# Performance work log

Measured on AMD Instinct MI355X. Metric: run time of the kernel, lower is better.

The kernel has to match this reference:

```python
import jax, jax.numpy as jnp
import numpy as np

N_HEAD = 16
HEAD_DIM = 64
R_VALUE = 256
EPS_LN = 1e-5


def _orf(x, omega, b):
    # orthogonal random features: sqrt(2/r) * cos(x @ omega.T + b)
    r = b.shape[0]
    return jnp.sqrt(2.0 / r) * jnp.cos(x @ omega.T + b)


def _layernorm(x, gamma, beta):
    m = jnp.mean(x, axis=-1, keepdims=True)
    v = jnp.var(x, axis=-1, keepdims=True)
    return (x - m) / jnp.sqrt(v + EPS_LN) * gamma + beta


def setup_inputs() -> dict:
    key = jax.random.key(0)
    ks = jax.random.split(key, 12)
    B, L = 4, 2048
    dm = N_HEAD * HEAD_DIM  # 1024
    inp = {}
    inp["pre_query"] = jax.random.normal(ks[0], (B, L, dm), jnp.float32)
    inp["pre_key"] = jax.random.normal(ks[1], (B, L, dm), jnp.float32)
    inp["pre_value"] = jax.random.normal(ks[2], (B, L, dm), jnp.float32)
    inp["wq"] = jax.random.normal(ks[3], (dm, dm), jnp.float32) * 0.02
    inp["wk"] = jax.random.normal(ks[4], (dm, dm), jnp.float32) * 0.02
    inp["wv"] = jax.random.normal(ks[5], (dm, dm), jnp.float32) * 0.02
    inp["wo"] = jax.random.normal(ks[6], (dm, dm), jnp.float32) * 0.02
    inp["gamma"] = jnp.ones((dm,), jnp.float32)
    inp["beta"] = jnp.zeros((dm,), jnp.float32)
    G = jax.random.normal(ks[7], (R_VALUE, HEAD_DIM), jnp.float32)
    omega, _ = jnp.linalg.qr(G)  # (r, head_dim), orthonormal columns
    inp["omega"] = omega
    inp["b"] = jax.random.uniform(ks[8], (R_VALUE,), jnp.float32) * 2.0 * jnp.pi
    return inp


def reference(pre_query, pre_key, pre_value, wq, wk, wv, wo, gamma, beta, omega, b):
    B, L, dm = pre_query.shape
    H, D = N_HEAD, dm // N_HEAD
    q = (pre_query @ wq.T).reshape(B, L, H, D)
    k = (pre_key @ wk.T).reshape(B, L, H, D)
    v = (pre_value @ wv.T).reshape(B, L, H, D)

    qp = _orf(q, omega, b)  # (B,L,H,R)
    kp = _orf(k, omega, b)  # (B,L,H,R)

    # causal Performer attention as a linear-attention recurrence:
    # S_t = S_{t-1} + k'_t v_t^T ; z_t = z_{t-1} + k'_t
    # out_t = (q'_t . S_t) / clamp(q'_t . z_t)
    R = b.shape[0]
    S0 = jnp.zeros((B, H, R, D), qp.dtype)
    z0 = jnp.zeros((B, H, R), qp.dtype)

    def step(carry, xs):
        S, z = carry
        q_t, k_t, v_t = xs  # (B,H,R),(B,H,R),(B,H,D)
        S = S + k_t[..., :, None] * v_t[..., None, :]
        z = z + k_t
        num = jnp.einsum('bhr,bhrd->bhd', q_t, S)
        den = jnp.clip(jnp.einsum('bhr,bhr->bh', q_t, z), 1e-6, None)
        return (S, z), num / (den[..., None] + 1e-6)

    xs = (qp.transpose(1, 0, 2, 3), kp.transpose(1, 0, 2, 3), v.transpose(1, 0, 2, 3))
    _, out = jax.lax.scan(step, (S0, z0), xs)  # (L,B,H,D)
    out = out.transpose(1, 0, 2, 3).reshape(B, L, dm)

    pre_result = out @ wo.T
    return _layernorm(pre_result + pre_query, gamma, beta)
```

## Files before the change

kernel.cpp:

```cpp
#include <hip/hip_runtime.h>
#include <hip/hip_bf16.h>


typedef float f4 __attribute__((ext_vector_type(4)));
typedef __attribute__((ext_vector_type(8))) short bf16x8;
typedef __attribute__((ext_vector_type(4))) float f32x4;
typedef unsigned short u16x4 __attribute__((ext_vector_type(4)));
typedef unsigned short u16x8 __attribute__((ext_vector_type(8)));

#define B_  4
#define L_  2048
#define H_  16
#define D_  64
#define DM_ 1024
#define R_  256
#define C_  64
#define NC_ (L_ / C_)
#define M_  (B_ * L_)
#define M2_ (M_ * H_)

static __device__ __forceinline__ unsigned short f2bu(float x) {
    __hip_bfloat16 h = __float2bfloat16(x);
    return *(unsigned short*)&h;
}
static __device__ __forceinline__ float bu2f(unsigned short u) {
    union { unsigned int i; float f; } c; c.i = ((unsigned int)u) << 16; return c.f;
}

typedef __attribute__((address_space(3))) void lds_void_t;
typedef __attribute__((address_space(1))) const void gvoid_t;
static __device__ __forceinline__ void gload16(const void* g, void* l) {
    __builtin_amdgcn_global_load_lds((gvoid_t*)g, (lds_void_t*)l, 16, 0, 0);
}

__launch_bounds__(256)
__global__ void cvt_bf16(const float* __restrict__ in, unsigned short* __restrict__ out, int n4) {
    int i = blockIdx.x * 256 + threadIdx.x;
    if (i < n4) {
        f4 v = *(const f4*)&in[(size_t)i * 4];
        ushort4 o;
        o.x = f2bu(v[0]); o.y = f2bu(v[1]); o.z = f2bu(v[2]); o.w = f2bu(v[3]);
        *(ushort4*)&out[(size_t)i * 4] = o;
    }
}

__launch_bounds__(256)
__global__ void cvt_bf16_x3(const float* __restrict__ i0, const float* __restrict__ i1,
                            const float* __restrict__ i2,
                            unsigned short* __restrict__ o0, unsigned short* __restrict__ o1,
                            unsigned short* __restrict__ o2, int n4) {
    const int z = blockIdx.z;
    const float* in = (z == 0) ? i0 : (z == 1) ? i1 : i2;
    unsigned short* out = (z == 0) ? o0 : (z == 1) ? o1 : o2;
    int i = blockIdx.x * 256 + threadIdx.x;
    if (i < n4) {
        f4 v = *(const f4*)&in[(size_t)i * 4];
        ushort4 o;
        o.x = f2bu(v[0]); o.y = f2bu(v[1]); o.z = f2bu(v[2]); o.w = f2bu(v[3]);
        *(ushort4*)&out[(size_t)i * 4] = o;
    }
}

__launch_bounds__(512)
__global__ void gemm_mfma_b3(const unsigned short* __restrict__ A0, const unsigned short* __restrict__ A1,
                             const unsigned short* __restrict__ A2,
                             const unsigned short* __restrict__ B0, const unsigned short* __restrict__ B1,
                             const unsigned short* __restrict__ B2,
                             unsigned short* __restrict__ C0, unsigned short* __restrict__ C1,
                             unsigned short* __restrict__ C2,
                             int M, int N, int K) {
    __shared__ unsigned short Asl[2][256 * 32];
    __shared__ unsigned short Bsl[2][256 * 32];
    const int z = blockIdx.z;
    const unsigned short* A  = (z == 0) ? A0 : (z == 1) ? A1 : A2;
    const unsigned short* Bw = (z == 0) ? B0 : (z == 1) ? B1 : B2;
    unsigned short*       Cb = (z == 0) ? C0 : (z == 1) ? C1 : C2;
    const int t = threadIdx.x;
    const int lane = t & 63, w = t >> 6;
    const int wr = w >> 2, wc = w & 3;
    const int nwg = gridDim.x * gridDim.y;
    const int bid = blockIdx.y * gridDim.x + blockIdx.x;
    const int cpx = nwg >> 3;
    const int swz = (bid & 7) * cpx + (bid >> 3);
    const int row0 = (swz / gridDim.x) * 256, col0 = (swz % gridDim.x) * 256;
    const int sr0 = t >> 2;
    const int ssw = (((t & 3) ^ ((t >> 3) & 3)) * 8);
    const int lg = lane >> 4, lr = lane & 15;
    const int aslot = (lg ^ ((lr >> 1) & 3)) * 8;

#define STAGE_B3(buf, kkk) do { \
        gload16(&A [(size_t)(row0 + sr0)       * K + (kkk) + ssw], &Asl[buf][t * 8]); \
        gload16(&A [(size_t)(row0 + sr0 + 128) * K + (kkk) + ssw], &Asl[buf][(t + 512) * 8]); \
        gload16(&Bw[(size_t)(col0 + sr0)       * K + (kkk) + ssw], &Bsl[buf][t * 8]); \
        gload16(&Bw[(size_t)(col0 + sr0 + 128) * K + (kkk) + ssw], &Bsl[buf][(t + 512) * 8]); \
    } while (0)

    f32x4 acc[8][4] = {};
    STAGE_B3(0, 0);
    int cur = 0;
    for (int kk = 0; kk < K; kk += 32) {
        if (kk + 32 < K) {
            STAGE_B3(cur ^ 1, kk + 32);
            asm volatile("s_waitcnt vmcnt(4)" ::: "memory");
        } else {
            asm volatile("s_waitcnt vmcnt(0)" ::: "memory");
        }
        __builtin_amdgcn_sched_barrier(0);
        __builtin_amdgcn_s_barrier();
        bf16x8 af[8], bfr[4];
#pragma unroll
        for (int m = 0; m < 8; ++m)
            af[m] = *(const bf16x8*)&Asl[cur][(wr * 128 + m * 16 + lr) * 32 + aslot];
#pragma unroll
        for (int n = 0; n < 4; ++n)
            bfr[n] = *(const bf16x8*)&Bsl[cur][(wc * 64 + n * 16 + lr) * 32 + aslot];
        __builtin_amdgcn_s_setprio(1);
#pragma unroll
        for (int m = 0; m < 8; ++m)
#pragma unroll
            for (int n = 0; n < 4; ++n)
                acc[m][n] = __builtin_amdgcn_mfma_f32_16x16x32_bf16(af[m], bfr[n], acc[m][n], 0, 0, 0);
        __builtin_amdgcn_s_setprio(0);
        __builtin_amdgcn_s_barrier();
        cur ^= 1;
    }
#undef STAGE_B3
#pragma unroll
    for (int m = 0; m < 8; ++m)
#pragma unroll
        for (int n = 0; n < 4; ++n)
#pragma unroll
            for (int i = 0; i < 4; ++i) {
                int r  = row0 + wr * 128 + m * 16 + lg * 4 + i;
                int cc = col0 + wc * 64 + n * 16 + lr;
                Cb[(size_t)r * N + cc] = f2bu(acc[m][n][i]);
            }
}

__launch_bounds__(256)
__global__ void gemm_out(const unsigned short* __restrict__ A,
                         const unsigned short* __restrict__ Bw,
                         const float* __restrict__ resid,
                         float* __restrict__ Cf,
                         int M, int N, int K) {
    __shared__ unsigned short Asl[3][64 * 32];
    __shared__ unsigned short Bsl[3][128 * 32];
    const int t = threadIdx.x;
    const int lane = t & 63, w = t >> 6;
    const int nwg = gridDim.x * gridDim.y;
    const int bid = blockIdx.y * gridDim.x + blockIdx.x;
    const int cpx = nwg >> 3;
    const int swz = (bid & 7) * cpx + (bid >> 3);
    const int row0 = (swz / gridDim.x) * 64, col0 = (swz % gridDim.x) * 128;
    const int sr0 = t >> 2;
    const int ssw = (((t & 3) ^ ((t >> 3) & 3)) * 8);
    const int lg = lane >> 4, lr = lane & 15;
    const int aslot = (lg ^ ((lr >> 1) & 3)) * 8;

#define STAGE_O(buf, kkk) do { \
        gload16(&A [(size_t)(row0 + sr0)      * K + (kkk) + ssw], &Asl[buf][t * 8]); \
        gload16(&Bw[(size_t)(col0 + sr0)      * K + (kkk) + ssw], &Bsl[buf][t * 8]); \
        gload16(&Bw[(size_t)(col0 + sr0 + 64) * K + (kkk) + ssw], &Bsl[buf][(t + 256) * 8]); \
    } while (0)
#define COMPUTE_O(buf) do { \
        bf16x8 af[4], bfr[2]; \
        _Pragma("unroll") \
        for (int m = 0; m < 4; ++m) \
            af[m] = *(const bf16x8*)&Asl[buf][(m * 16 + lr) * 32 + aslot]; \
        _Pragma("unroll") \
        for (int n = 0; n < 2; ++n) \
            bfr[n] = *(const bf16x8*)&Bsl[buf][(w * 32 + n * 16 + lr) * 32 + aslot]; \
        _Pragma("unroll") \
        for (int m = 0; m < 4; ++m) \
            _Pragma("unroll") \
            for (int n = 0; n < 2; ++n) \
                acc[m][n] = __builtin_amdgcn_mfma_f32_16x16x32_bf16(af[m], bfr[n], acc[m][n], 0, 0, 0); \
    } while (0)

    f32x4 acc[4][2] = {};
    STAGE_O(0, 0);
    STAGE_O(1, 32);
    int cur = 0;
    for (int kk = 0; kk + 64 < K; kk += 32) {
        int nx = cur + 2; if (nx >= 3) nx -= 3;
        STAGE_O(nx, kk + 64);
        asm volatile("s_waitcnt vmcnt(6)" ::: "memory");
        __builtin_amdgcn_sched_barrier(0);
        __builtin_amdgcn_s_barrier();
        COMPUTE_O(cur);
        __builtin_amdgcn_s_barrier();
        cur = (cur == 2) ? 0 : cur + 1;
    }
    asm volatile("s_waitcnt vmcnt(3)" ::: "memory");
    __builtin_amdgcn_sched_barrier(0);
    __builtin_amdgcn_s_barrier();
    COMPUTE_O(cur);
    __builtin_amdgcn_s_barrier();
    cur = (cur == 2) ? 0 : cur + 1;
    asm volatile("s_waitcnt vmcnt(0)" ::: "memory");
    __builtin_amdgcn_sched_barrier(0);
    __builtin_amdgcn_s_barrier();
    COMPUTE_O(cur);
#undef STAGE_O
#undef COMPUTE_O
#pragma unroll
    for (int m = 0; m < 4; ++m)
#pragma unroll
        for (int n = 0; n < 2; ++n)
#pragma unroll
            for (int i = 0; i < 4; ++i) {
                int r  = row0 + m * 16 + lg * 4 + i;
                int cc = col0 + w * 32 + n * 16 + lr;
                size_t off = (size_t)r * N + cc;
                Cf[off] = acc[m][n][i] + resid[off];
            }
}

#define RS_STRIDE 272
__launch_bounds__(256)
__global__ void feat_mfma_b2(const unsigned short* __restrict__ X0, const unsigned short* __restrict__ X1,
                             const unsigned short* __restrict__ om,
                             const float* __restrict__ bvec,
                             unsigned short* __restrict__ O0, unsigned short* __restrict__ O1) {
    __shared__ unsigned short Xs[2 * 64 * 32];
    __shared__ unsigned short Pool[64 * RS_STRIDE];
    const int z = blockIdx.z;
    const unsigned short* X = z ? X1 : X0;
    unsigned short* out = z ? O1 : O0;
    const int t = threadIdx.x;
    const int lane = t & 63, w = t >> 6;
    const int lg = lane >> 4, lr = lane & 15;
    const int m0 = blockIdx.x * 64;
    const int aslot = (lg ^ ((lr >> 1) & 3)) * 8;

#pragma unroll
    for (int i = 0; i < 2; ++i) {
        int cch = i * 256 + t;
        int ks = cch >> 8, row = (cch >> 2) & 63;
        int sub = ((cch & 3) ^ ((cch >> 3) & 3)) * 8;
        gload16(&X[(size_t)(m0 + row) * 64 + ks * 32 + sub], &Xs[cch * 8]);
    }
#pragma unroll
    for (int i = 0; i < 8; ++i) {
        int cch = i * 256 + t;
        int ks = cch >> 10, r = (cch >> 2) & 255;
        int sub = ((cch & 3) ^ ((cch >> 3) & 3)) * 8;
        gload16(&om[(size_t)r * 64 + ks * 32 + sub], &Pool[cch * 8]);
    }
    __syncthreads();

    f32x4 acc[4][4] = {};
#pragma unroll
    for (int ks = 0; ks < 2; ++ks) {
        bf16x8 af[4], bfr[4];
#pragma unroll
        for (int m = 0; m < 4; ++m)
            af[m] = *(const bf16x8*)&Xs[ks * 2048 + (m * 16 + lr) * 32 + aslot];
#pragma unroll
        for (int n = 0; n < 4; ++n)
            bfr[n] = *(const bf16x8*)&Pool[ks * 8192 + (w * 64 + n * 16 + lr) * 32 + aslot];
#pragma unroll
        for (int m = 0; m < 4; ++m)
#pragma unroll
            for (int n = 0; n < 4; ++n)
                acc[m][n] = __builtin_amdgcn_mfma_f32_16x16x32_bf16(af[m], bfr[n], acc[m][n], 0, 0, 0);
    }
    __syncthreads();

    const float scale = 0.08838834764831845f;
#pragma unroll
    for (int n = 0; n < 4; ++n) {
        const int col = w * 64 + n * 16 + lr;
        const float bb = bvec[col];
#pragma unroll
        for (int m = 0; m < 4; ++m)
#pragma unroll
            for (int ii = 0; ii < 4; ++ii)
                Pool[(m * 16 + lg * 4 + ii) * RS_STRIDE + col] = f2bu(scale * __cosf(acc[m][n][ii] + bb));
    }
    __syncthreads();
#pragma unroll
    for (int i = 0; i < 8; ++i) {
        int cch = i * 256 + t;
        int row = cch >> 5, colc = (cch & 31) * 8;
        u16x8 vv = *(const u16x8*)&Pool[row * RS_STRIDE + colc];
        *(u16x8*)&out[(size_t)(m0 + row) * 256 + colc] = vv;
    }
}

__launch_bounds__(256)
__global__ void passA_mfma(const unsigned short* __restrict__ kp, const unsigned short* __restrict__ vb,
                           unsigned short* __restrict__ kvT, float* __restrict__ ksum) {
    __shared__ __align__(16) unsigned short KPt[256][72];
    __shared__ __align__(16) unsigned short Vt[64][72];
    const int c = blockIdx.x, h = blockIdx.y, bz = blockIdx.z;
    const int t = threadIdx.x;
    const int lane = t & 63, w = t >> 6;
    const int lg = lane >> 4, lr = lane & 15;
    const int l0 = c * C_;
    const int bh = bz * H_ + h;

    {
        const int l4 = (t & 15) * 4, rs = (t >> 4) * 16;
        u16x8 row[4][2];
#pragma unroll
        for (int i = 0; i < 4; ++i) {
            const unsigned short* src = &kp[((size_t)(bz * L_ + l0 + l4 + i) * H_ + h) * R_ + rs];
            row[i][0] = *(const u16x8*)src;
            row[i][1] = *(const u16x8*)(src + 8);
        }
#pragma unroll
        for (int q = 0; q < 16; ++q) {
            u16x4 pk = { row[0][q >> 3][q & 7], row[1][q >> 3][q & 7],
                         row[2][q >> 3][q & 7], row[3][q >> 3][q & 7] };
            *(u16x4*)&KPt[rs + q][l4] = pk;
        }
    }
    {
        const int d4 = (t & 15) * 4, ls = (t >> 4) * 4;
        u16x4 x[4];
#pragma unroll
        for (int i = 0; i < 4; ++i)
            x[i] = *(const u16x4*)&vb[(size_t)(bz * L_ + l0 + ls + i) * DM_ + h * 64 + d4];
#pragma unroll
        for (int q = 0; q < 4; ++q) {
            u16x4 pk = { x[0][q], x[1][q], x[2][q], x[3][q] };
            *(u16x4*)&Vt[d4 + q][ls] = pk;
        }
    }
    __syncthreads();

    f32x4 acc[4][4] = {};
#pragma unroll
    for (int ks = 0; ks < 2; ++ks) {
        bf16x8 af[4], bfr[4];
#pragma unroll
        for (int m = 0; m < 4; ++m)
            af[m] = *(const bf16x8*)&KPt[64 * w + 16 * m + lr][ks * 32 + lg * 8];
#pragma unroll
        for (int n = 0; n < 4; ++n)
            bfr[n] = *(const bf16x8*)&Vt[16 * n + lr][ks * 32 + lg * 8];
#pragma unroll
        for (int m = 0; m < 4; ++m)
#pragma unroll
            for (int n = 0; n < 4; ++n)
                acc[m][n] = __builtin_amdgcn_mfma_f32_16x16x32_bf16(af[m], bfr[n], acc[m][n], 0, 0, 0);
    }
    size_t sbase = ((size_t)(bh * NC_ + c)) * 64 * R_;
#pragma unroll
    for (int n = 0; n < 4; ++n)
#pragma unroll
        for (int m = 0; m < 4; ++m) {
            int d = 16 * n + lr;
            int r = 64 * w + 16 * m + lg * 4;
            u16x4 pk = { f2bu(acc[m][n][0]), f2bu(acc[m][n][1]),
                         f2bu(acc[m][n][2]), f2bu(acc[m][n][3]) };
            *(u16x4*)&kvT[sbase + (size_t)d * R_ + r] = pk;
        }
    {
        float s = 0.f;
#pragma unroll
        for (int j = 0; j < 8; ++j) {
            u16x8 vv = *(const u16x8*)&KPt[t][j * 8];
#pragma unroll
            for (int q = 0; q < 8; ++q) s += bu2f(vv[q]);
        }
        ksum[((size_t)(bh * NC_ + c)) * R_ + t] = s;
    }
}

__launch_bounds__(256)
__global__ void passB_chain(unsigned short* __restrict__ kvT, float* __restrict__ ksum) {
    const int bx = blockIdx.x, h = blockIdx.y, bz = blockIdx.z;
    const int t = threadIdx.x;
    const int bh = bz * H_ + h;
    const int idx = bx * 256 + t;
    const int d = idx >> 6;
    const int rg = (idx & 63) * 4;
    size_t base = ((size_t)bh * NC_ * 64 + d) * R_ + rg;
    const size_t cstride = (size_t)64 * R_;
    float run0 = 0.f, run1 = 0.f, run2 = 0.f, run3 = 0.f;
    for (int c = 0; c < NC_; ++c) {
        size_t ix = base + (size_t)c * cstride;
        u16x4 v = *(const u16x4*)&kvT[ix];
        u16x4 o = { f2bu(run0), f2bu(run1), f2bu(run2), f2bu(run3) };
        *(u16x4*)&kvT[ix] = o;
        run0 += bu2f(v[0]); run1 += bu2f(v[1]);
        run2 += bu2f(v[2]); run3 += bu2f(v[3]);
    }
    if (bx == 0) {
        float rz = 0.f;
        for (int c = 0; c < NC_; ++c) {
            size_t ix = ((size_t)bh * NC_ + c) * R_ + t;
            float tmp = ksum[ix];
            ksum[ix] = rz;
            rz += tmp;
        }
    }
}

__launch_bounds__(256)
__global__ void passC_mfma(const unsigned short* __restrict__ qp, const unsigned short* __restrict__ kp,
                           const unsigned short* __restrict__ vb, const unsigned short* __restrict__ kvT,
                           const float* __restrict__ zpref, unsigned short* __restrict__ attnb) {
    __shared__ __align__(16) unsigned short Sl[64 * 256];
    __shared__ __align__(16) unsigned short Vt[80][72];
    __shared__ __align__(16) unsigned short As[64][72];

    const int c = blockIdx.x, h = blockIdx.y, bz = blockIdx.z;
    const int t = threadIdx.x;
    const int lane = t & 63, w = t >> 6;
    const int lg = lane >> 4, lr = lane & 15;
    const int l0 = c * C_;
    const int bh = bz * H_ + h;
    const size_t sbase = ((size_t)(bh * NC_ + c)) * 64 * R_;
    const size_t zbase = ((size_t)(bh * NC_ + c)) * R_;

#pragma unroll
    for (int i = 0; i < 8; ++i) {
        int idx = i * 256 + t;
        int row = idx >> 5, s = idx & 31;
        gload16(&kvT[sbase + (size_t)row * R_ + ((s ^ (row & 7)) << 3)], &Sl[idx * 8]);
    }

    {
        const int d4 = (t & 15) * 4, ls = (t >> 4) * 4;
        u16x4 x[4];
#pragma unroll
        for (int i = 0; i < 4; ++i)
            x[i] = *(const u16x4*)&vb[(size_t)(bz * L_ + l0 + ls + i) * DM_ + h * 64 + d4];
#pragma unroll
        for (int q = 0; q < 4; ++q) {
            u16x4 pk = { x[0][q], x[1][q], x[2][q], x[3][q] };
            *(u16x4*)&Vt[d4 + q][ls] = pk;
        }
    }
    if (t < 16) {
        u16x4 ones = { 0x3F80, 0x3F80, 0x3F80, 0x3F80 };
        *(u16x4*)&Vt[64][t * 4] = ones;
    }

    const size_t qrow = ((size_t)(bz * L_ + l0 + 16 * w + lr) * H_ + h) * R_;
    bf16x8 aq[8];
#pragma unroll
    for (int ks = 0; ks < 8; ++ks) aq[ks] = *(const bf16x8*)&qp[qrow + ks * 32 + lg * 8];

    f32x4 sacc[4] = {};
#pragma unroll
    for (int half = 0; half < 2; ++half) {
        bf16x8 bk[4][4];
#pragma unroll
        for (int k2 = 0; k2 < 4; ++k2)
#pragma unroll
            for (int n = 0; n < 4; ++n)
                bk[k2][n] = *(const bf16x8*)&kp[((size_t)(bz * L_ + l0 + 16 * n + lr) * H_ + h) * R_
                                                + (half * 4 + k2) * 32 + lg * 8];
        __builtin_amdgcn_s_setprio(1);
#pragma unroll
        for (int k2 = 0; k2 < 4; ++k2)
#pragma unroll
            for (int n = 0; n < 4; ++n)
                sacc[n] = __builtin_amdgcn_mfma_f32_16x16x32_bf16(aq[half * 4 + k2], bk[k2][n], sacc[n], 0, 0, 0);
        __builtin_amdgcn_s_setprio(0);
    }
#pragma unroll
    for (int n = 0; n < 4; ++n)
#pragma unroll
        for (int ii = 0; ii < 4; ++ii) {
            int i_loc = 16 * w + lg * 4 + ii;
            int j_loc = 16 * n + lr;
            As[i_loc][j_loc] = (j_loc <= i_loc) ? f2bu(sacc[n][ii]) : (unsigned short)0;
        }

    u16x8 zu[8];
#pragma unroll
    for (int ks = 0; ks < 8; ++ks) {
        f4 z0 = *(const f4*)&zpref[zbase + ks * 32 + lg * 8];
        f4 z1 = *(const f4*)&zpref[zbase + ks * 32 + lg * 8 + 4];
        zu[ks] = u16x8{ f2bu(z0[0]), f2bu(z0[1]), f2bu(z0[2]), f2bu(z0[3]),
                        f2bu(z1[0]), f2bu(z1[1]), f2bu(z1[2]), f2bu(z1[3]) };
    }
    __syncthreads();

    f32x4 oacc[4] = {};
    f32x4 dacc = {};
    __builtin_amdgcn_s_setprio(1);
#pragma unroll
    for (int ks = 0; ks < 8; ++ks) {
#pragma unroll
        for (int n = 0; n < 4; ++n) {
            int row = 16 * n + lr;
            int slot = (ks * 4 + lg) ^ (lr & 7);
            bf16x8 bs = *(const bf16x8*)&Sl[row * 256 + slot * 8];
            oacc[n] = __builtin_amdgcn_mfma_f32_16x16x32_bf16(aq[ks], bs, oacc[n], 0, 0, 0);
        }
        dacc = __builtin_amdgcn_mfma_f32_16x16x32_bf16(aq[ks], *(bf16x8*)&zu[ks], dacc, 0, 0, 0);
    }

    f32x4 racc = {};
#pragma unroll
    for (int ks = 0; ks < 2; ++ks) {
        bf16x8 aa = *(const bf16x8*)&As[16 * w + lr][ks * 32 + lg * 8];
#pragma unroll
        for (int n = 0; n < 4; ++n) {
            bf16x8 bv = *(const bf16x8*)&Vt[16 * n + lr][ks * 32 + lg * 8];
            oacc[n] = __builtin_amdgcn_mfma_f32_16x16x32_bf16(aa, bv, oacc[n], 0, 0, 0);
        }
        bf16x8 b4 = *(const bf16x8*)&Vt[64 + lr][ks * 32 + lg * 8];
        racc = __builtin_amdgcn_mfma_f32_16x16x32_bf16(aa, b4, racc, 0, 0, 0);
    }
    __builtin_amdgcn_s_setprio(0);

#pragma unroll
    for (int ii = 0; ii < 4; ++ii) {
        float rs_ = __shfl(racc[ii], lane & 48, 64);
        float den = rs_ + dacc[ii];
        float inv = 1.f / (fmaxf(den, 1e-6f) + 1e-6f);
#pragma unroll
        for (int n = 0; n < 4; ++n)
            attnb[(size_t)(bz * L_ + l0 + 16 * w + lg * 4 + ii) * DM_ + h * 64 + 16 * n + lr] =
                f2bu(oacc[n][ii] * inv);
    }
}

__launch_bounds__(256)
__global__ void ln_kernel(float* __restrict__ io, const float* __restrict__ gamma,
                          const float* __restrict__ beta) {
    __shared__ float wsum[4], wsum2[4];
    const int row = blockIdx.x;
    const int t = threadIdx.x;
    f4 x = *(const f4*)&io[(size_t)row * DM_ + t * 4];
    float s  = x[0] + x[1] + x[2] + x[3];
    float s2 = x[0]*x[0] + x[1]*x[1] + x[2]*x[2] + x[3]*x[3];
#pragma unroll
    for (int o = 32; o > 0; o >>= 1) {
        s  += __shfl_down(s, o);
        s2 += __shfl_down(s2, o);
    }
    if ((t & 63) == 0) { wsum[t >> 6] = s; wsum2[t >> 6] = s2; }
    __syncthreads();
    s  = wsum[0]  + wsum[1]  + wsum[2]  + wsum[3];
    s2 = wsum2[0] + wsum2[1] + wsum2[2] + wsum2[3];
    const float m = s * (1.f / DM_);
    const float var = s2 * (1.f / DM_) - m * m;
    const float rstd = rsqrtf(var + 1e-5f);
    f4 g  = *(const f4*)&gamma[t * 4];
    f4 bb = *(const f4*)&beta[t * 4];
    f4 o = (x - m) * rstd * g + bb;
    *(f4*)&io[(size_t)row * DM_ + t * 4] = o;
}

extern "C" void kernel_launch(void* const* d_in, const int* in_sizes, int n_in,
                              void* d_out, int out_size, void* d_ws, size_t ws_size,
                              hipStream_t stream) {
    const float* pre_q = (const float*)d_in[0];
    const float* pre_k = (const float*)d_in[1];
    const float* pre_v = (const float*)d_in[2];
    const float* wq    = (const float*)d_in[3];
    const float* wk    = (const float*)d_in[4];
    const float* wv    = (const float*)d_in[5];
    const float* wo    = (const float*)d_in[6];
    const float* gamma = (const float*)d_in[7];
    const float* beta  = (const float*)d_in[8];
    const float* omega = (const float*)d_in[9];
    const float* bvec  = (const float*)d_in[10];

    const size_t NEED = 226ull << 20;
    if (ws_size < NEED) return;

    char* w = (char*)d_ws;
    unsigned short* qp    = (unsigned short*)(w);
    unsigned short* kp    = (unsigned short*)(w + (64ull << 20));
    unsigned short* kvT   = (unsigned short*)(w + (128ull << 20));
    unsigned short* vb    = (unsigned short*)(w + (192ull << 20));
    unsigned short* attnb = (unsigned short*)(w + (208ull << 20));
    float*          ksum  = (float*)(w + (224ull << 20));
    unsigned short* aq    = (unsigned short*)(w);
    unsigned short* ak    = (unsigned short*)(w + (16ull << 20));
    unsigned short* av    = (unsigned short*)(w + (32ull << 20));
    unsigned short* wq_bf = (unsigned short*)(w + (48ull << 20));
    unsigned short* wk_bf = (unsigned short*)(w + (50ull << 20));
    unsigned short* wv_bf = (unsigned short*)(w + (52ull << 20));
    unsigned short* qx    = (unsigned short*)(w + (128ull << 20));
    unsigned short* kx    = (unsigned short*)(w + (144ull << 20));
    unsigned short* om_bf = (unsigned short*)(w + (208ull << 20));
    unsigned short* wo_bf = (unsigned short*)(w + (64ull << 20));
    float*          outb  = (float*)d_out;

    const int n4_big = M_ * DM_ / 4;
    const int n4_w   = DM_ * DM_ / 4;
    const int n4_om  = R_ * D_ / 4;
    dim3 gg3(DM_ / 256, M_ / 256, 3);
    dim3 ggo(DM_ / 128, M_ / 64);

    cvt_bf16_x3<<<dim3((n4_big + 255) / 256, 1, 3), 256, 0, stream>>>(
        pre_q, pre_k, pre_v, aq, ak, av, n4_big);
    cvt_bf16_x3<<<dim3((n4_w + 255) / 256, 1, 3), 256, 0, stream>>>(
        wq, wk, wv, wq_bf, wk_bf, wv_bf, n4_w);
    cvt_bf16<<<(n4_om + 255) / 256, 256, 0, stream>>>(omega, om_bf, n4_om);

    gemm_mfma_b3<<<gg3, 512, 0, stream>>>(aq, ak, av, wq_bf, wk_bf, wv_bf,
                                          qx, kx, vb, M_, DM_, DM_);
    feat_mfma_b2<<<dim3(M2_ / 64, 1, 2), 256, 0, stream>>>(qx, kx, om_bf, bvec, qp, kp);

    passA_mfma<<<dim3(NC_, H_, B_), 256, 0, stream>>>(kp, vb, kvT, ksum);
    passB_chain<<<dim3(16, H_, B_), 256, 0, stream>>>(kvT, ksum);
    passC_mfma<<<dim3(NC_, H_, B_), 256, 0, stream>>>(qp, kp, vb, kvT, ksum, attnb);

    cvt_bf16<<<(n4_w + 255) / 256, 256, 0, stream>>>(wo, wo_bf, n4_w);
    gemm_out<<<ggo, 256, 0, stream>>>(attnb, wo_bf, pre_q, outb, M_, DM_, DM_);
    ln_kernel<<<M_, 256, 0, stream>>>(outb, gamma, beta);
}
```

Measured before the change: 316.8 us.

## Fuse fp32-to-bf16 input conversion into the QKV projection GEMM

Drops the separate conversion pass that wrote bf16 copies of the three activation inputs. The QKV GEMM now loads fp32 activations into registers, converts them, and writes them to LDS itself, while the weights still arrive through direct global-to-LDS loads. The tile shrinks from 256x256 with 512 threads to 128x128 with 256 threads. This removes a full read and write of roughly 100MB of activations, at the cost of doubling the activation bytes read inside the GEMM, register staging, and smaller tiles with less reuse.

```diff
diff --git a/kernel.cpp b/kernel.cpp
--- a/kernel.cpp
+++ b/kernel.cpp
@@ -61,77 +61,92 @@
     }
 }
 
-__launch_bounds__(512)
-__global__ void gemm_mfma_b3(const unsigned short* __restrict__ A0, const unsigned short* __restrict__ A1,
-                             const unsigned short* __restrict__ A2,
-                             const unsigned short* __restrict__ B0, const unsigned short* __restrict__ B1,
-                             const unsigned short* __restrict__ B2,
-                             unsigned short* __restrict__ C0, unsigned short* __restrict__ C1,
-                             unsigned short* __restrict__ C2,
-                             int M, int N, int K) {
-    __shared__ unsigned short Asl[2][256 * 32];
-    __shared__ unsigned short Bsl[2][256 * 32];
+__launch_bounds__(256)
+__global__ void gemm_qkv(const float* __restrict__ A0, const float* __restrict__ A1,
+                         const float* __restrict__ A2,
+                         const unsigned short* __restrict__ B0, const unsigned short* __restrict__ B1,
+                         const unsigned short* __restrict__ B2,
+                         unsigned short* __restrict__ C0, unsigned short* __restrict__ C1,
+                         unsigned short* __restrict__ C2,
+                         int M, int N, int K) {
+    __shared__ unsigned short Asl[2][128 * 32];
+    __shared__ unsigned short Bsl[2][128 * 32];
     const int z = blockIdx.z;
-    const unsigned short* A  = (z == 0) ? A0 : (z == 1) ? A1 : A2;
+    const float* A = (z == 0) ? A0 : (z == 1) ? A1 : A2;
     const unsigned short* Bw = (z == 0) ? B0 : (z == 1) ? B1 : B2;
     unsigned short*       Cb = (z == 0) ? C0 : (z == 1) ? C1 : C2;
     const int t = threadIdx.x;
     const int lane = t & 63, w = t >> 6;
-    const int wr = w >> 2, wc = w & 3;
+    const int wr = w >> 1, wc = w & 1;
     const int nwg = gridDim.x * gridDim.y;
     const int bid = blockIdx.y * gridDim.x + blockIdx.x;
     const int cpx = nwg >> 3;
     const int swz = (bid & 7) * cpx + (bid >> 3);
-    const int row0 = (swz / gridDim.x) * 256, col0 = (swz % gridDim.x) * 256;
+    const int row0 = (swz / gridDim.x) * 128, col0 = (swz % gridDim.x) * 128;
     const int sr0 = t >> 2;
     const int ssw = (((t & 3) ^ ((t >> 3) & 3)) * 8);
     const int lg = lane >> 4, lr = lane & 15;
     const int aslot = (lg ^ ((lr >> 1) & 3)) * 8;
 
-#define STAGE_B3(buf, kkk) do { \
-        gload16(&A [(size_t)(row0 + sr0)       * K + (kkk) + ssw], &Asl[buf][t * 8]); \
-        gload16(&A [(size_t)(row0 + sr0 + 128) * K + (kkk) + ssw], &Asl[buf][(t + 512) * 8]); \
-        gload16(&Bw[(size_t)(col0 + sr0)       * K + (kkk) + ssw], &Bsl[buf][t * 8]); \
-        gload16(&Bw[(size_t)(col0 + sr0 + 128) * K + (kkk) + ssw], &Bsl[buf][(t + 512) * 8]); \
+#define LOADA(kkk) do { \
+        ar0 = *(const f4*)&A[(size_t)(row0 + sr0)      * K + (kkk) + ssw]; \
+        ar1 = *(const f4*)&A[(size_t)(row0 + sr0)      * K + (kkk) + ssw + 4]; \
+        ar2 = *(const f4*)&A[(size_t)(row0 + sr0 + 64) * K + (kkk) + ssw]; \
+        ar3 = *(const f4*)&A[(size_t)(row0 + sr0 + 64) * K + (kkk) + ssw + 4]; \
     } while (0)
-
-    f32x4 acc[8][4] = {};
-    STAGE_B3(0, 0);
+#define WRITEA(buf) do { \
+        u16x8 w0 = { f2bu(ar0[0]), f2bu(ar0[1]), f2bu(ar0[2]), f2bu(ar0[3]), \
+                     f2bu(ar1[0]), f2bu(ar1[1]), f2bu(ar1[2]), f2bu(ar1[3]) }; \
+        u16x8 w1 = { f2bu(ar2[0]), f2bu(ar2[1]), f2bu(ar2[2]), f2bu(ar2[3]), \
+                     f2bu(ar3[0]), f2bu(ar3[1]), f2bu(ar3[2]), f2bu(ar3[3]) }; \
+        *(u16x8*)&Asl[buf][t * 8] = w0; \
+        *(u16x8*)&Asl[buf][(t + 256) * 8] = w1; \
+    } while (0)
+#define STAGEB(buf, kkk) do { \
+        gload16(&Bw[(size_t)(col0 + sr0)      * K + (kkk) + ssw], &Bsl[buf][t * 8]); \
+        gload16(&Bw[(size_t)(col0 + sr0 + 64) * K + (kkk) + ssw], &Bsl[buf][(t + 256) * 8]); \
+    } while (0)
+
+    f32x4 acc[4][4] = {};
+    f4 ar0, ar1, ar2, ar3;
+    LOADA(0);
+    STAGEB(0, 0);
+    WRITEA(0);
+    __syncthreads();
     int cur = 0;
     for (int kk = 0; kk < K; kk += 32) {
         if (kk + 32 < K) {
-            STAGE_B3(cur ^ 1, kk + 32);
-            asm volatile("s_waitcnt vmcnt(4)" ::: "memory");
-        } else {
-            asm volatile("s_waitcnt vmcnt(0)" ::: "memory");
-        }
-        __builtin_amdgcn_sched_barrier(0);
-        __builtin_amdgcn_s_barrier();
-        bf16x8 af[8], bfr[4];
-#pragma unroll
-        for (int m = 0; m < 8; ++m)
-            af[m] = *(const bf16x8*)&Asl[cur][(wr * 128 + m * 16 + lr) * 32 + aslot];
+            LOADA(kk + 32);
+            STAGEB(cur ^ 1, kk + 32);
+        }
+        bf16x8 af[4], bfr[4];
+#pragma unroll
+        for (int m = 0; m < 4; ++m)
+            af[m] = *(const bf16x8*)&Asl[cur][(wr * 64 + m * 16 + lr) * 32 + aslot];
 #pragma unroll
         for (int n = 0; n < 4; ++n)
             bfr[n] = *(const bf16x8*)&Bsl[cur][(wc * 64 + n * 16 + lr) * 32 + aslot];
         __builtin_amdgcn_s_setprio(1);
 #pragma unroll
-        for (int m = 0; m < 8; ++m)
+        for (int m = 0; m < 4; ++m)
 #pragma unroll
             for (int n = 0; n < 4; ++n)
                 acc[m][n] = __builtin_amdgcn_mfma_f32_16x16x32_bf16(af[m], bfr[n], acc[m][n], 0, 0, 0);
         __builtin_amdgcn_s_setprio(0);
-        __builtin_amdgcn_s_barrier();
+        if (kk + 32 < K) WRITEA(cur ^ 1);
+        __syncthreads();
         cur ^= 1;
     }
-#undef STAGE_B3
-#pragma unroll
-    for (int m = 0; m < 8; ++m)
+#undef LOADA
+#undef WRITEA
+#undef STAGEB
+#pragma unroll
+    for (int m = 0; m < 4; ++m)
 #pragma unroll
         for (int n = 0; n < 4; ++n)
 #pragma unroll
             for (int i = 0; i < 4; ++i) {
-                int r  = row0 + wr * 128 + m * 16 + lg * 4 + i;
+                int r  = row0 + wr * 64 + m * 16 + lg * 4 + i;
                 int cc = col0 + wc * 64 + n * 16 + lr;
                 Cb[(size_t)r * N + cc] = f2bu(acc[m][n][i]);
             }
@@ -575,32 +590,26 @@
     unsigned short* vb    = (unsigned short*)(w + (192ull << 20));
     unsigned short* attnb = (unsigned short*)(w + (208ull << 20));
     float*          ksum  = (float*)(w + (224ull << 20));
-    unsigned short* aq    = (unsigned short*)(w);
-    unsigned short* ak    = (unsigned short*)(w + (16ull << 20));
-    unsigned short* av    = (unsigned short*)(w + (32ull << 20));
-    unsigned short* wq_bf = (unsigned short*)(w + (48ull << 20));
-    unsigned short* wk_bf = (unsigned short*)(w + (50ull << 20));
-    unsigned short* wv_bf = (unsigned short*)(w + (52ull << 20));
+    unsigned short* wq_bf = (unsigned short*)(w);
+    unsigned short* wk_bf = (unsigned short*)(w + (2ull << 20));
+    unsigned short* wv_bf = (unsigned short*)(w + (4ull << 20));
     unsigned short* qx    = (unsigned short*)(w + (128ull << 20));
     unsigned short* kx    = (unsigned short*)(w + (144ull << 20));
     unsigned short* om_bf = (unsigned short*)(w + (208ull << 20));
     unsigned short* wo_bf = (unsigned short*)(w + (64ull << 20));
     float*          outb  = (float*)d_out;
 
-    const int n4_big = M_ * DM_ / 4;
     const int n4_w   = DM_ * DM_ / 4;
     const int n4_om  = R_ * D_ / 4;
-    dim3 gg3(DM_ / 256, M_ / 256, 3);
+    dim3 gg3(DM_ / 128, M_ / 128, 3);
     dim3 ggo(DM_ / 128, M_ / 64);
 
-    cvt_bf16_x3<<<dim3((n4_big + 255) / 256, 1, 3), 256, 0, stream>>>(
-        pre_q, pre_k, pre_v, aq, ak, av, n4_big);
     cvt_bf16_x3<<<dim3((n4_w + 255) / 256, 1, 3), 256, 0, stream>>>(
         wq, wk, wv, wq_bf, wk_bf, wv_bf, n4_w);
     cvt_bf16<<<(n4_om + 255) / 256, 256, 0, stream>>>(omega, om_bf, n4_om);
 
-    gemm_mfma_b3<<<gg3, 512, 0, stream>>>(aq, ak, av, wq_bf, wk_bf, wv_bf,
-                                          qx, kx, vb, M_, DM_, DM_);
+    gemm_qkv<<<gg3, 256, 0, stream>>>(pre_q, pre_k, pre_v, wq_bf, wk_bf, wv_bf,
+                                      qx, kx, vb, M_, DM_, DM_);
     feat_mfma_b2<<<dim3(M2_ / 64, 1, 2), 256, 0, stream>>>(qx, kx, om_bf, bvec, qp, kp);
 
     passA_mfma<<<dim3(NC_, H_, B_), 256, 0, stream>>>(kp, vb, kvT, ksum);
```

After: 299.5 us. 5.5% less time.
